# Kernel optimization log

Measured on AMD Instinct MI355X. Metric: run time of the kernel, lower is better.

The kernel has to match this reference:

```python
import jax, jax.numpy as jnp
import numpy as np

ALPHA = 0.2  # leaky_relu negative slope (init arg `alpha`)


def setup_inputs() -> dict:
    key = jax.random.key(0)
    k0, k1, k2, k3, k4 = jax.random.split(key, 5)
    B, N, F_IN, F_OUT, H = 8, 512, 128, 64, 1  # n_heads must be 1 (torch.cat constraint)
    h = jax.random.normal(k0, (B, N, F_IN), jnp.float32)
    edge_features = jax.random.normal(k1, (B, N, N, F_OUT), jnp.float32)
    # learned params (xavier-ish scale)
    W = jax.random.normal(k2, (H, F_IN, F_OUT), jnp.float32) * 0.1
    U = jax.random.normal(k3, (H, F_OUT), jnp.float32) * 0.1
    a = jax.random.normal(k4, (H, 2 * F_OUT + 1), jnp.float32) * 0.1
    return {"h": h, "edge_features": edge_features, "W": W, "U": U, "a": a}


def reference(h, edge_features, W, U, a):
    # h: [B,N,F_in], edge_features: [B,N,N,F_out], W: [H,F_in,F_out], U: [H,F_out], a: [H,2*F_out+1]
    F_OUT = W.shape[-1]
    Wh = jnp.einsum('bni,hio->bhno', h, W)  # [B,H,N,F_out]
    # Split additive attention vector instead of materializing the O(N^2, 2F+1) concat:
    # sum(cat([Wh_i, Wh_j, edge_t]) * a) == Wh_i@a_i + Wh_j@a_j + edge_t*a_e
    a_i = a[:, :F_OUT]            # [H,F_out]
    a_j = a[:, F_OUT:2 * F_OUT]   # [H,F_out]
    a_e = a[:, 2 * F_OUT]         # [H]
    e_i = jnp.einsum('bhno,ho->bhn', Wh, a_i)  # score contribution of node i
    e_j = jnp.einsum('bhno,ho->bhn', Wh, a_j)  # score contribution of node j
    edge_s = jnp.einsum('bijo,ho->bhij', edge_features, U)  # [B,H,N,N] (H=1)
    e = e_i[:, :, :, None] + e_j[:, :, None, :] + edge_s * a_e[None, :, None, None]
    e = jnp.where(e >= 0, e, ALPHA * e)  # leaky_relu
    attn = jax.nn.softmax(e, axis=3)     # softmax over neighbors j (dropout p=0 -> identity)
    h_prime = jnp.einsum('bhij,bhjo->bhio', attn, Wh)  # [B,H,N,F_out]
    B, H, N, _ = h_prime.shape
    # concat=True: [B,N,H*F_out]
    return jnp.transpose(h_prime, (0, 2, 1, 3)).reshape(B, N, H * F_OUT)
```

## Files before the change

kernel.cpp:

```cpp
#include <hip/hip_runtime.h>

#define BN 8
#define NN 512
#define FIN 128
#define FOUT 64
#define ALPHA 0.2f

__global__ __launch_bounds__(64) void wh_kernel(
    const float* __restrict__ h, const float* __restrict__ W,
    const float* __restrict__ a,
    float* __restrict__ Wh, float* __restrict__ e_i, float* __restrict__ e_j) {
    int bn = blockIdx.x;
    int o  = threadIdx.x;
    __shared__ float hrow[FIN];
    hrow[o]      = h[bn * FIN + o];
    hrow[o + 64] = h[bn * FIN + 64 + o];
    __syncthreads();
    float acc = 0.f;
#pragma unroll 8
    for (int i = 0; i < FIN; ++i)
        acc = fmaf(hrow[i], W[i * FOUT + o], acc);
    Wh[bn * FOUT + o] = acc;
    float pi = acc * a[o];
    float pj = acc * a[FOUT + o];
#pragma unroll
    for (int off = 32; off >= 1; off >>= 1) {
        pi += __shfl_xor(pi, off, 64);
        pj += __shfl_xor(pj, off, 64);
    }
    if (o == 0) { e_i[bn] = pi; e_j[bn] = pj; }
}

__global__ __launch_bounds__(256) void attn_kernel(
    const float* __restrict__ edge, const float* __restrict__ U,
    const float* __restrict__ a, const float* __restrict__ Wh,
    const float* __restrict__ e_i, const float* __restrict__ e_j,
    float* __restrict__ out) {
    int bi   = blockIdx.x;
    int b    = bi >> 9;
    int tid  = threadIdx.x;
    int lane = tid & 63;
    int wave = tid >> 6;

    __shared__ float s_lds[NN];
    __shared__ float ej_lds[NN];
    __shared__ float red[8];
    __shared__ float accbuf[4][FOUT];

    ej_lds[tid]       = e_j[(b << 9) + tid];
    ej_lds[tid + 256] = e_j[(b << 9) + tid + 256];

    float a_e = a[2 * FOUT];
    float eiv = e_i[bi];
    int   sub = lane & 15;
    float4 Uv = ((const float4*)U)[sub];
    const float4* erow = (const float4*)(edge + (size_t)bi * (NN * FOUT));
    int jbase = (wave << 2) + (lane >> 4);
    __syncthreads();

#pragma unroll 4
    for (int it = 0; it < 32; ++it) {
        int j = (it << 4) + jbase;
        float4 ef = erow[(j << 4) + sub];
        float p = ef.x * Uv.x + ef.y * Uv.y + ef.z * Uv.z + ef.w * Uv.w;
        p += __shfl_xor(p, 8, 16);
        p += __shfl_xor(p, 4, 16);
        p += __shfl_xor(p, 2, 16);
        p += __shfl_xor(p, 1, 16);
        if (sub == 0) {
            float s = eiv + ej_lds[j] + a_e * p;
            s_lds[j] = (s >= 0.f) ? s : (ALPHA * s);
        }
    }
    __syncthreads();

    float m = fmaxf(s_lds[tid], s_lds[tid + 256]);
#pragma unroll
    for (int off = 32; off >= 1; off >>= 1) m = fmaxf(m, __shfl_xor(m, off, 64));
    if (lane == 0) red[wave] = m;
    __syncthreads();
    m = fmaxf(fmaxf(red[0], red[1]), fmaxf(red[2], red[3]));
    float v0 = expf(s_lds[tid] - m);
    float v1 = expf(s_lds[tid + 256] - m);
    float ssum = v0 + v1;
    s_lds[tid] = v0;
    s_lds[tid + 256] = v1;
#pragma unroll
    for (int off = 32; off >= 1; off >>= 1) ssum += __shfl_xor(ssum, off, 64);
    if (lane == 0) red[4 + wave] = ssum;
    __syncthreads();
    float inv = 1.0f / (red[4] + red[5] + red[6] + red[7]);

    int o = tid & 63, chunk = tid >> 6;
    const float* WhB = Wh + (((size_t)b) << 9) * FOUT;
    float acc = 0.f;
    int j0 = chunk << 7;
#pragma unroll 8
    for (int j = j0; j < j0 + 128; ++j)
        acc = fmaf(s_lds[j], WhB[(j << 6) + o], acc);
    accbuf[chunk][o] = acc;
    __syncthreads();
    if (chunk == 0) {
        float r = (accbuf[0][o] + accbuf[1][o] + accbuf[2][o] + accbuf[3][o]) * inv;
        out[((size_t)bi << 6) + o] = r;
    }
}

extern "C" void kernel_launch(void* const* d_in, const int* in_sizes, int n_in,
                              void* d_out, int out_size, void* d_ws, size_t ws_size,
                              hipStream_t stream) {
    const float* h    = (const float*)d_in[0];
    const float* edge = (const float*)d_in[1];
    const float* W    = (const float*)d_in[2];
    const float* U    = (const float*)d_in[3];
    const float* a    = (const float*)d_in[4];
    float* out = (float*)d_out;

    float* Wh  = (float*)d_ws;
    float* e_i = Wh + BN * NN * FOUT;
    float* e_j = e_i + BN * NN;

    wh_kernel<<<BN * NN, 64, 0, stream>>>(h, W, a, Wh, e_i, e_j);
    attn_kernel<<<BN * NN, 256, 0, stream>>>(edge, U, a, Wh, e_i, e_j, out);
}
```

Baseline: 700.3 us.

## Split attention into a streaming score kernel and a softmax-matvec kernel

Splits the fused attention kernel in two. A score kernel streams the edge features over twice as many blocks and writes leaky-relu scores to a workspace buffer, and a separate kernel does the softmax and the weighted sum over Wh. This is meant to raise parallelism and memory-level concurrency on the dominant edge-feature read (about 537 MB), which used to be serialized with the softmax and matvec phases in each block. The cost is an extra launch and a workspace round trip of about 8 MB of scores.

New measurement: 718.9 us. 2.7% more time.

```diff
diff --git a/kernel.cpp b/kernel.cpp
--- a/kernel.cpp
+++ b/kernel.cpp
@@ -31,10 +31,47 @@
     if (o == 0) { e_i[bn] = pi; e_j[bn] = pj; }
 }
 
-__global__ __launch_bounds__(256) void attn_kernel(
+__global__ __launch_bounds__(256) void score_kernel(
     const float* __restrict__ edge, const float* __restrict__ U,
-    const float* __restrict__ a, const float* __restrict__ Wh,
+    const float* __restrict__ a,
     const float* __restrict__ e_i, const float* __restrict__ e_j,
+    float* __restrict__ sws) {
+    int idx  = blockIdx.x;
+    int bi   = idx >> 1;
+    int half = idx & 1;
+    int b    = bi >> 9;
+    int tid  = threadIdx.x;
+    int lane = tid & 63;
+    int wave = tid >> 6;
+    int sub  = lane & 15;
+
+    float4 Uv  = ((const float4*)U)[sub];
+    float  a_e = a[2 * FOUT];
+    float  eiv = e_i[bi];
+    const float4* erow = (const float4*)(edge + (size_t)bi * (NN * FOUT));
+    const float*  ejb  = e_j + (b << 9);
+    float*        srow = sws + (size_t)bi * NN;
+
+    int jofs = (half << 8) + (wave << 2) + (lane >> 4);
+#pragma unroll 8
+    for (int it = 0; it < 16; ++it) {
+        int j = (it << 4) + jofs;
+        float4 ef = erow[(j << 4) + sub];
+        float p = fmaf(ef.x, Uv.x, fmaf(ef.y, Uv.y, fmaf(ef.z, Uv.z, ef.w * Uv.w)));
+        p += __shfl_xor(p, 1, 16);
+        p += __shfl_xor(p, 2, 16);
+        p += __shfl_xor(p, 4, 16);
+        p += __shfl_xor(p, 8, 16);
+        float s = eiv + ejb[j] + a_e * p;
+        s = (s >= 0.f) ? s : (ALPHA * s);
+        float v = __shfl(s, (lane & 3) << 4, 64);
+        if (lane < 4)
+            srow[(it << 4) + (half << 8) + (wave << 2) + lane] = v;
+    }
+}
+
+__global__ __launch_bounds__(256) void soft_mv_kernel(
+    const float* __restrict__ sws, const float* __restrict__ Wh,
     float* __restrict__ out) {
     int bi   = blockIdx.x;
     int b    = bi >> 9;
@@ -42,49 +79,25 @@
     int lane = tid & 63;
     int wave = tid >> 6;
 
-    __shared__ float s_lds[NN];
-    __shared__ float ej_lds[NN];
+    __shared__ float p_lds[NN];
     __shared__ float red[8];
     __shared__ float accbuf[4][FOUT];
 
-    ej_lds[tid]       = e_j[(b << 9) + tid];
-    ej_lds[tid + 256] = e_j[(b << 9) + tid + 256];
+    const float* srow = sws + (size_t)bi * NN;
+    float s0 = srow[tid];
+    float s1 = srow[tid + 256];
 
-    float a_e = a[2 * FOUT];
-    float eiv = e_i[bi];
-    int   sub = lane & 15;
-    float4 Uv = ((const float4*)U)[sub];
-    const float4* erow = (const float4*)(edge + (size_t)bi * (NN * FOUT));
-    int jbase = (wave << 2) + (lane >> 4);
-    __syncthreads();
-
-#pragma unroll 4
-    for (int it = 0; it < 32; ++it) {
-        int j = (it << 4) + jbase;
-        float4 ef = erow[(j << 4) + sub];
-        float p = ef.x * Uv.x + ef.y * Uv.y + ef.z * Uv.z + ef.w * Uv.w;
-        p += __shfl_xor(p, 8, 16);
-        p += __shfl_xor(p, 4, 16);
-        p += __shfl_xor(p, 2, 16);
-        p += __shfl_xor(p, 1, 16);
-        if (sub == 0) {
-            float s = eiv + ej_lds[j] + a_e * p;
-            s_lds[j] = (s >= 0.f) ? s : (ALPHA * s);
-        }
-    }
-    __syncthreads();
-
-    float m = fmaxf(s_lds[tid], s_lds[tid + 256]);
+    float m = fmaxf(s0, s1);
 #pragma unroll
     for (int off = 32; off >= 1; off >>= 1) m = fmaxf(m, __shfl_xor(m, off, 64));
     if (lane == 0) red[wave] = m;
     __syncthreads();
     m = fmaxf(fmaxf(red[0], red[1]), fmaxf(red[2], red[3]));
-    float v0 = expf(s_lds[tid] - m);
-    float v1 = expf(s_lds[tid + 256] - m);
+    float v0 = expf(s0 - m);
+    float v1 = expf(s1 - m);
     float ssum = v0 + v1;
-    s_lds[tid] = v0;
-    s_lds[tid + 256] = v1;
+    p_lds[tid]       = v0;
+    p_lds[tid + 256] = v1;
 #pragma unroll
     for (int off = 32; off >= 1; off >>= 1) ssum += __shfl_xor(ssum, off, 64);
     if (lane == 0) red[4 + wave] = ssum;
@@ -97,7 +110,7 @@
     int j0 = chunk << 7;
 #pragma unroll 8
     for (int j = j0; j < j0 + 128; ++j)
-        acc = fmaf(s_lds[j], WhB[(j << 6) + o], acc);
+        acc = fmaf(p_lds[j], WhB[(j << 6) + o], acc);
     accbuf[chunk][o] = acc;
     __syncthreads();
     if (chunk == 0) {
@@ -119,7 +132,9 @@
     float* Wh  = (float*)d_ws;
     float* e_i = Wh + BN * NN * FOUT;
     float* e_j = e_i + BN * NN;
+    float* sws = e_j + BN * NN;
 
     wh_kernel<<<BN * NN, 64, 0, stream>>>(h, W, a, Wh, e_i, e_j);
-    attn_kernel<<<BN * NN, 256, 0, stream>>>(edge, U, a, Wh, e_i, e_j, out);
+    score_kernel<<<BN * NN * 2, 256, 0, stream>>>(edge, U, a, e_i, e_j, sws);
+    soft_mv_kernel<<<BN * NN, 256, 0, stream>>>(sws, Wh, out);
 }
```
